# Kernel tuning notes

Hardware: AMD Instinct MI355X
Metric: run time of the kernel (lower is better)

## Reference

```python
import jax, jax.numpy as jnp
import numpy as np

N = 50000   # nodes
E = 800000  # edges
IN = 128
H = 256
OUT = 10
G = 128     # graphs in batch


def _uniform(key, shape, fan_in):
    bound = 1.0 / np.sqrt(fan_in)
    return jax.random.uniform(key, shape, jnp.float32, -bound, bound)


def setup_inputs() -> dict:
    key = jax.random.key(0)
    ks = jax.random.split(key, 12)
    x = jax.random.normal(ks[0], (N, IN), jnp.float32)
    edge_index = jax.random.randint(ks[1], (2, E), 0, N, dtype=jnp.int64)
    edge_weight = jax.random.uniform(ks[2], (E,), jnp.float32)
    batch = jnp.sort(jax.random.randint(ks[3], (N,), 0, G, dtype=jnp.int64))
    # GCNConv weights (bias=False)
    W0 = _uniform(ks[4], (IN, H), IN)
    W1 = _uniform(ks[5], (H, H), H)
    W2 = _uniform(ks[6], (H, H), H)
    # MLP head: [H, H, OUT]
    Wm1 = _uniform(ks[7], (H, H), H)
    bm1 = _uniform(ks[8], (H,), H)
    Wm2 = _uniform(ks[9], (H, OUT), H)
    bm2 = _uniform(ks[10], (OUT,), H)
    return dict(x=x, edge_index=edge_index, edge_weight=edge_weight, batch=batch,
                W0=W0, W1=W1, W2=W2, Wm1=Wm1, bm1=bm1, Wm2=Wm2, bm2=bm2)


def _gcn_conv(h, W, row, col, dinv_sqrt):
    """GCNConv with self-loops and symmetric deg^-1/2 normalization, bias=False.
    Self-loop contribution handled analytically (norm = dinv_sqrt[i]^2)."""
    hw = h @ W                                        # [N, H]
    norm = dinv_sqrt[row] * dinv_sqrt[col]            # [E]
    msg = hw[row] * norm[:, None]                     # [E, H] gather-scale
    agg = jax.ops.segment_sum(msg, col, num_segments=N)  # scatter-add at targets
    return agg + (dinv_sqrt * dinv_sqrt)[:, None] * hw    # add self-loop term


def reference(x, edge_index, edge_weight, batch, W0, W1, W2, Wm1, bm1, Wm2, bm2):
    row, col = edge_index[0], edge_index[1]
    # degree including self-loop (edge_weight is ignored, as in the source)
    deg = jax.ops.segment_sum(jnp.ones((E,), x.dtype), col, num_segments=N) + 1.0
    dinv_sqrt = jax.lax.rsqrt(deg)
    h = x
    for W in (W0, W1, W2):
        h = jax.nn.relu(_gcn_conv(h, W, row, col, dinv_sqrt))
    # global mean pool over graphs
    counts = jax.ops.segment_sum(jnp.ones((N,), h.dtype), batch, num_segments=G)
    pooled = jax.ops.segment_sum(h, batch, num_segments=G) / jnp.maximum(counts, 1.0)[:, None]
    # MLP head (dropout inactive at inference)
    hmid = jax.nn.relu(pooled @ Wm1 + bm1)
    last = hmid @ Wm2 + bm2
    return jax.nn.log_softmax(last, axis=-1), jax.nn.sigmoid(last), last
```

## Files before the change

### kernel.cpp

```cpp
#include <hip/hip_runtime.h>
#include <math.h>

#define N_NODES 50000
#define N_PAD   50048
#define N_EDGES 800000
#define CSR_CAP 1200000
#define IN_F 128
#define H_F 256
#define OUT_F 10
#define N_G 128
#define POOL_CHUNK 128
#define POOL_MAXCHUNKS 16
#define NCHUNKS 196

typedef __attribute__((ext_vector_type(4))) float f32x4;
typedef __attribute__((ext_vector_type(2))) float f32x2;
typedef unsigned char u8;

__device__ inline f32x2 fp8x2_f32_lo(unsigned int v) {
    return __builtin_amdgcn_cvt_pk_f32_fp8(v, false);
}
__device__ inline f32x2 fp8x2_f32_hi(unsigned int v) {
    return __builtin_amdgcn_cvt_pk_f32_fp8(v, true);
}
__device__ inline unsigned int f32_fp8x2_lo(float a, float b, unsigned int old) {
    return __builtin_amdgcn_cvt_pk_fp8_f32(a, b, old, false);
}
__device__ inline unsigned int f32_fp8x2_hi(float a, float b, unsigned int old) {
    return __builtin_amdgcn_cvt_pk_fp8_f32(a, b, old, true);
}
__device__ inline u8 f32_fp8(float a) {
    return (u8)(f32_fp8x2_lo(a, a, 0u) & 0xff);
}
__device__ inline ushort f2bf(float x) {
    union { float f; unsigned int u; } v; v.f = x;
    unsigned int r = v.u + 0x7fff + ((v.u >> 16) & 1);
    return (ushort)(r >> 16);
}
__device__ inline float bf2f(ushort u) {
    union { unsigned int u; float f; } v; v.u = ((unsigned int)u) << 16; return v.f;
}

__device__ inline void gl2lds16(const void* g, void* l) {
    __builtin_amdgcn_global_load_lds(
        (const __attribute__((address_space(1))) unsigned int*)g,
        (__attribute__((address_space(3))) unsigned int*)l,
        16, 0, 0);
}

#define PREP_HIST 782
#define PREP_X   (PREP_HIST + 6250)
#define PREP_T0  (PREP_X + 128)
#define PREP_T1  (PREP_T0 + 256)
#define PREP_T2  (PREP_T1 + 256)
#define PREP_GS  (PREP_T2 + NCHUNKS)

__global__ __launch_bounds__(256) void prep_kernel(
    const int* __restrict__ col, int* __restrict__ counts,
    int* __restrict__ rank,
    const float* __restrict__ x, u8* __restrict__ xb,
    const float* __restrict__ W0, u8* __restrict__ W0t,
    const float* __restrict__ W1, u8* __restrict__ W1t,
    const float* __restrict__ W2, u8* __restrict__ W2t,
    const int* __restrict__ batch, int* __restrict__ gstart) {
    int b = blockIdx.x;
    int tid = threadIdx.x;
    if (b < PREP_HIST) {
        int base = b * 1024 + tid;
        int c[4];
        #pragma unroll
        for (int u = 0; u < 4; ++u) {
            int e = base + u * 256;
            c[u] = (e < N_EDGES) ? col[e] : -1;
        }
        int rk[4];
        #pragma unroll
        for (int u = 0; u < 4; ++u)
            if (c[u] >= 0) rk[u] = atomicAdd(&counts[c[u]], 1);
        #pragma unroll
        for (int u = 0; u < 4; ++u)
            if (c[u] >= 0) rank[base + u * 256] = rk[u];
    } else if (b < PREP_X) {
        int i = (b - PREP_HIST) * 256 + tid;
        float4 v = *(const float4*)(x + (size_t)i * 4);
        unsigned int p = f32_fp8x2_lo(v.x, v.y, 0u);
        p = f32_fp8x2_hi(v.z, v.w, p);
        *(unsigned int*)(xb + (size_t)i * 4) = p;
    } else if (b < PREP_T0) {
        int idx = (b - PREP_X) * 256 + tid;
        int k = idx >> 8, nn = idx & 255;
        W0t[nn * IN_F + k] = f32_fp8(W0[idx]);
    } else if (b < PREP_T1) {
        int idx = (b - PREP_T0) * 256 + tid;
        int k = idx >> 8, nn = idx & 255;
        W1t[nn * H_F + k] = f32_fp8(W1[idx]);
    } else if (b < PREP_T2) {
        int idx = (b - PREP_T1) * 256 + tid;
        int k = idx >> 8, nn = idx & 255;
        W2t[nn * H_F + k] = f32_fp8(W2[idx]);
    } else {
        int i = (b - PREP_T2) * 256 + tid;
        if (i >= N_NODES) return;
        int bb = batch[i];
        if (i == 0) {
            for (int g = 0; g <= bb; ++g) gstart[g] = 0;
        } else {
            int p = batch[i - 1];
            if (p != bb) { for (int g = p + 1; g <= bb; ++g) gstart[g] = i; }
        }
        if (i == N_NODES - 1) {
            for (int g = bb + 1; g <= N_G; ++g) gstart[g] = N_NODES;
        }
    }
}

__global__ __launch_bounds__(256) void chunk_reduce(const int* __restrict__ counts,
                                                    int* __restrict__ csum,
                                                    float* __restrict__ pooled, int n) {
    if (blockIdx.x < 128) pooled[blockIdx.x * 256 + threadIdx.x] = 0.f;
    int i = blockIdx.x * 256 + threadIdx.x;
    int v = (i < n) ? ((counts[i] + 7) & ~7) : 0;
    #pragma unroll
    for (int off = 32; off; off >>= 1) v += __shfl_down(v, off);
    __shared__ int ws[4];
    if ((threadIdx.x & 63) == 0) ws[threadIdx.x >> 6] = v;
    __syncthreads();
    if (threadIdx.x == 0) csum[blockIdx.x] = ws[0] + ws[1] + ws[2] + ws[3];
}

__global__ __launch_bounds__(256) void scan_dinv_kernel(const int* __restrict__ counts,
                                                        const int* __restrict__ csum,
                                                        int* __restrict__ offsets,
                                                        float* __restrict__ dinv,
                                                        unsigned int* __restrict__ csr_ew,
                                                        int n) {
    int tid = threadIdx.x;
    int lane = tid & 63, wid = tid >> 6;
    int cv = (tid < NCHUNKS) ? csum[tid] : 0;
    int xc = cv;
    #pragma unroll
    for (int off = 1; off < 64; off <<= 1) {
        int t = __shfl_up(xc, off);
        if (lane >= off) xc += t;
    }
    __shared__ int cw[4], cpre[4];
    __shared__ int cexcl[257];
    if (lane == 63) cw[wid] = xc;
    __syncthreads();
    if (tid == 0) { int s = 0; for (int k = 0; k < 4; ++k) { cpre[k] = s; s += cw[k]; } }
    __syncthreads();
    cexcl[tid] = cpre[wid] + xc - cv;
    if (tid == 255) cexcl[256] = cpre[3] + cw[3];
    __syncthreads();
    int base = cexcl[blockIdx.x];
    int i = blockIdx.x * 256 + tid;
    int v = (i < n) ? counts[i] : 0;
    int pv = (v + 7) & ~7;
    int x = pv;
    #pragma unroll
    for (int off = 1; off < 64; off <<= 1) {
        int t = __shfl_up(x, off);
        if (lane >= off) x += t;
    }
    __shared__ int wsum[4], wpre[4];
    if (lane == 63) wsum[wid] = x;
    __syncthreads();
    if (tid == 0) { int s = 0; for (int k = 0; k < 4; ++k) { wpre[k] = s; s += wsum[k]; } }
    __syncthreads();
    if (i < n) {
        int o = base + wpre[wid] + x - pv;
        offsets[i] = o;
        dinv[i] = rsqrtf((float)(v + 1));
        for (int z = v; z < pv; ++z) csr_ew[o + z] = 0u;
    }
    if (blockIdx.x == 0 && tid == 0) offsets[n] = cexcl[NCHUNKS];
}

__global__ __launch_bounds__(256) void fill_csr_kernel(const int* __restrict__ row,
                                                       const int* __restrict__ col,
                                                       const int* __restrict__ offsets,
                                                       const int* __restrict__ rank,
                                                       const float* __restrict__ dinv,
                                                       unsigned int* __restrict__ csr_ew) {
    int e0 = blockIdx.x * 512 + threadIdx.x;
    int e1 = e0 + 256;
    int c0 = -1, c1 = -1, r0 = 0, r1 = 0, k0 = 0, k1 = 0;
    if (e0 < N_EDGES) { c0 = col[e0]; r0 = row[e0]; k0 = rank[e0]; }
    if (e1 < N_EDGES) { c1 = col[e1]; r1 = row[e1]; k1 = rank[e1]; }
    float dc0 = 0.f, dr0 = 0.f, dc1 = 0.f, dr1 = 0.f;
    if (c0 >= 0) { dc0 = dinv[c0]; dr0 = dinv[r0]; }
    if (c1 >= 0) { dc1 = dinv[c1]; dr1 = dinv[r1]; }
    if (c0 >= 0)
        csr_ew[offsets[c0] + k0] = (unsigned int)r0 | ((unsigned int)f2bf(dc0 * dr0) << 16);
    if (c1 >= 0)
        csr_ew[offsets[c1] + k1] = (unsigned int)r1 | ((unsigned int)f2bf(dc1 * dr1) << 16);
}

template <int K, bool RELU>
__global__ __launch_bounds__(256) void gemm_fp8(const u8* __restrict__ A,
                                                const u8* __restrict__ Bt,
                                                u8* __restrict__ C) {
    __shared__ u8 As[4 * 4096];
    __shared__ u8 Bs[4 * 4096];
    int tid = threadIdx.x;
    int lane = tid & 63;
    int w = tid >> 6;
    int wm = w & 1, wn = w >> 1;
    int l16 = lane & 15, quad = lane >> 4;
    int row0 = blockIdx.x * 128;
    int col0 = blockIdx.y * 128;
    f32x4 acc[4][4] = {};

    int sr = tid >> 1;
    int sh = (tid & 1) * 16;
    const u8* ga = A + (size_t)(row0 + sr) * K + sh;
    const u8* gb = Bt + (size_t)(col0 + sr) * K + sh;

    #pragma unroll
    for (int k0 = 0; k0 < K; k0 += 128) {
        if (k0) __syncthreads();
        #pragma unroll
        for (int q = 0; q < 4; ++q) {
            gl2lds16(ga + k0 + q * 32, As + q * 4096 + w * 1024);
            gl2lds16(gb + k0 + q * 32, Bs + q * 4096 + w * 1024);
        }
        __syncthreads();
        #pragma unroll
        for (int h = 0; h < 4; ++h) {
            long af[4], bfr[4];
            #pragma unroll
            for (int i = 0; i < 4; ++i)
                af[i] = *(const long*)&As[h * 4096 + (wm * 64 + i * 16 + l16) * 32 + quad * 8];
            #pragma unroll
            for (int j = 0; j < 4; ++j)
                bfr[j] = *(const long*)&Bs[h * 4096 + (wn * 64 + j * 16 + l16) * 32 + quad * 8];
            #pragma unroll
            for (int i = 0; i < 4; ++i)
                #pragma unroll
                for (int j = 0; j < 4; ++j)
                    acc[i][j] = __builtin_amdgcn_mfma_f32_16x16x32_fp8_fp8(af[i], bfr[j], acc[i][j], 0, 0, 0);
        }
    }
    #pragma unroll
    for (int i = 0; i < 4; ++i) {
        int rowb = row0 + wm * 64 + i * 16 + quad * 4;
        #pragma unroll
        for (int r = 0; r < 4; ++r) {
            int grow = rowb + r;
            #pragma unroll
            for (int j = 0; j < 4; ++j) {
                int gcol = col0 + wn * 64 + j * 16 + l16;
                float v = acc[i][j][r];
                if (RELU) v = fmaxf(v, 0.f);
                C[(size_t)grow * H_F + gcol] = f32_fp8(v);
            }
        }
    }
}

__global__ __launch_bounds__(256) void aggregate128(const u8* __restrict__ hw,
                                                    const float* __restrict__ dinv,
                                                    const int* __restrict__ offsets,
                                                    const unsigned int* __restrict__ csr_ew,
                                                    u8* __restrict__ hout) {
    int w = threadIdx.x >> 6;
    int lane = threadIdx.x & 63;
    int i = blockIdx.x * 4 + w;
    if (i >= N_NODES) return;
    float di = dinv[i];
    const u8* base = hw + (size_t)lane * 2;
    unsigned int su = *(const unsigned short*)(base + (size_t)i * IN_F);
    f32x2 sv = fp8x2_f32_lo(su);
    float s = di * di;
    float a0 = s * sv.x, a1 = s * sv.y;
    int t = __builtin_amdgcn_readfirstlane(offsets[i]);
    int end = __builtin_amdgcn_readfirstlane(offsets[i + 1]);
    if (t < end) {
        uint4 eA = *(const uint4*)(csr_ew + t);
        uint4 eB = *(const uint4*)(csr_ew + t + 4);
        for (; t < end; t += 8) {
            uint4 nA, nB;
            if (t + 8 < end) {
                nA = *(const uint4*)(csr_ew + t + 8);
                nB = *(const uint4*)(csr_ew + t + 12);
            }
            unsigned int e[8] = {eA.x, eA.y, eA.z, eA.w, eB.x, eB.y, eB.z, eB.w};
            unsigned int v[8];
            #pragma unroll
            for (int u = 0; u < 8; ++u)
                v[u] = *(const unsigned short*)(base + (size_t)(e[u] & 0xffff) * IN_F);
            #pragma unroll
            for (int u = 0; u < 8; ++u) {
                float wq = bf2f((ushort)(e[u] >> 16));
                f32x2 f = fp8x2_f32_lo(v[u]);
                a0 += wq * f.x; a1 += wq * f.y;
            }
            eA = nA; eB = nB;
        }
    }
    unsigned int o = f32_fp8x2_lo(a0, a1, 0u);
    *(unsigned short*)(hout + (size_t)i * IN_F + lane * 2) = (unsigned short)(o & 0xffff);
}

__global__ __launch_bounds__(256) void aggregate256(const u8* __restrict__ hw,
                                                    const float* __restrict__ dinv,
                                                    const int* __restrict__ offsets,
                                                    const unsigned int* __restrict__ csr_ew,
                                                    u8* __restrict__ hout) {
    int w = threadIdx.x >> 6;
    int lane = threadIdx.x & 63;
    int i = blockIdx.x * 4 + w;
    if (i >= N_NODES) return;
    float di = dinv[i];
    const u8* base = hw + (size_t)lane * 4;
    unsigned int su = *(const unsigned int*)(base + (size_t)i * H_F);
    f32x2 slo = fp8x2_f32_lo(su), shi = fp8x2_f32_hi(su);
    float s = di * di;
    float a0 = s * slo.x, a1 = s * slo.y, a2 = s * shi.x, a3 = s * shi.y;
    int t = __builtin_amdgcn_readfirstlane(offsets[i]);
    int end = __builtin_amdgcn_readfirstlane(offsets[i + 1]);
    if (t < end) {
        uint4 eA = *(const uint4*)(csr_ew + t);
        uint4 eB = *(const uint4*)(csr_ew + t + 4);
        for (; t < end; t += 8) {
            uint4 nA, nB;
            if (t + 8 < end) {
                nA = *(const uint4*)(csr_ew + t + 8);
                nB = *(const uint4*)(csr_ew + t + 12);
            }
            unsigned int e[8] = {eA.x, eA.y, eA.z, eA.w, eB.x, eB.y, eB.z, eB.w};
            unsigned int v[8];
            #pragma unroll
            for (int u = 0; u < 8; ++u)
                v[u] = *(const unsigned int*)(base + (size_t)(e[u] & 0xffff) * H_F);
            #pragma unroll
            for (int u = 0; u < 8; ++u) {
                float wq = bf2f((ushort)(e[u] >> 16));
                f32x2 lo = fp8x2_f32_lo(v[u]), hi = fp8x2_f32_hi(v[u]);
                a0 += wq * lo.x; a1 += wq * lo.y;
                a2 += wq * hi.x; a3 += wq * hi.y;
            }
            eA = nA; eB = nB;
        }
    }
    unsigned int o = f32_fp8x2_lo(fmaxf(a0, 0.f), fmaxf(a1, 0.f), 0u);
    o = f32_fp8x2_hi(fmaxf(a2, 0.f), fmaxf(a3, 0.f), o);
    *(unsigned int*)(hout + (size_t)i * H_F + lane * 4) = o;
}

__global__ __launch_bounds__(256) void pool_part(const u8* __restrict__ h,
                                                 const int* __restrict__ gstart,
                                                 float* __restrict__ pooled) {
    int g = blockIdx.x;
    int s = gstart[g] + blockIdx.y * POOL_CHUNK;
    int e = min(gstart[g + 1], s + POOL_CHUNK);
    if (s >= e) return;
    int w = threadIdx.x >> 6;
    int lane = threadIdx.x & 63;
    float a0 = 0.f, a1 = 0.f, a2 = 0.f, a3 = 0.f;
    for (int i = s + w; i < e; i += 4) {
        unsigned int v = *(const unsigned int*)(h + (size_t)i * H_F + lane * 4);
        f32x2 lo = fp8x2_f32_lo(v), hi = fp8x2_f32_hi(v);
        a0 += lo.x; a1 += lo.y; a2 += hi.x; a3 += hi.y;
    }
    __shared__ float sm[4][H_F];
    *(f32x4*)&sm[w][lane * 4] = (f32x4){a0, a1, a2, a3};
    __syncthreads();
    int t = threadIdx.x;
    float tot = sm[0][t] + sm[1][t] + sm[2][t] + sm[3][t];
    atomicAdd(&pooled[g * H_F + t], tot);
}

__global__ __launch_bounds__(256) void mlp_head_kernel(const float* __restrict__ pooled,
                                                       const int* __restrict__ gstart,
                                                       const float* __restrict__ Wm1,
                                                       const float* __restrict__ bm1,
                                                       const float* __restrict__ Wm2,
                                                       const float* __restrict__ bm2,
                                                       float* __restrict__ out) {
    __shared__ float p[H_F];
    __shared__ float h[H_F];
    __shared__ float lastv[OUT_F];
    __shared__ float stats[2];
    int g = blockIdx.x, j = threadIdx.x;
    int cnt = gstart[g + 1] - gstart[g];
    p[j] = pooled[g * H_F + j] / (float)max(cnt, 1);
    __syncthreads();
    float acc = bm1[j];
    for (int k = 0; k < H_F; ++k) acc += p[k] * Wm1[k * H_F + j];
    h[j] = fmaxf(acc, 0.f);
    __syncthreads();
    if (j < OUT_F) {
        float a = bm2[j];
        for (int k = 0; k < H_F; ++k) a += h[k] * Wm2[k * OUT_F + j];
        lastv[j] = a;
    }
    __syncthreads();
    if (j == 0) {
        float m = -1e30f;
        for (int o = 0; o < OUT_F; ++o) m = fmaxf(m, lastv[o]);
        float s = 0.f;
        for (int o = 0; o < OUT_F; ++o) s += expf(lastv[o] - m);
        stats[0] = m; stats[1] = logf(s);
    }
    __syncthreads();
    if (j < OUT_F) {
        float v = lastv[j];
        out[g * OUT_F + j] = v - stats[0] - stats[1];
        out[(size_t)N_G * OUT_F + g * OUT_F + j] = 1.f / (1.f + expf(-v));
        out[(size_t)2 * N_G * OUT_F + g * OUT_F + j] = v;
    }
}

extern "C" void kernel_launch(void* const* d_in, const int* in_sizes, int n_in,
                              void* d_out, int out_size, void* d_ws, size_t ws_size,
                              hipStream_t stream) {
    const float* x   = (const float*)d_in[0];
    const int* edge_index = (const int*)d_in[1];
    const int* batch = (const int*)d_in[3];
    const float* W0  = (const float*)d_in[4];
    const float* W1  = (const float*)d_in[5];
    const float* W2  = (const float*)d_in[6];
    const float* Wm1 = (const float*)d_in[7];
    const float* bm1 = (const float*)d_in[8];
    const float* Wm2 = (const float*)d_in[9];
    const float* bm2 = (const float*)d_in[10];
    float* out = (float*)d_out;

    char* ws = (char*)d_ws;
    size_t off = 0;
    auto alloc = [&](size_t bytes) -> void* {
        void* p = ws + off; off += (bytes + 255) & ~(size_t)255; return p;
    };
    u8* xb       = (u8*)alloc((size_t)N_PAD * IN_F);
    u8* bufA     = (u8*)alloc((size_t)N_PAD * H_F);
    u8* bufB     = (u8*)alloc((size_t)N_PAD * H_F);
    u8* t0       = (u8*)alloc((size_t)N_PAD * IN_F);
    u8* W0t      = (u8*)alloc((size_t)H_F * IN_F);
    u8* W1t      = (u8*)alloc((size_t)H_F * H_F);
    u8* W2t      = (u8*)alloc((size_t)H_F * H_F);
    float* dinv    = (float*)alloc((size_t)N_NODES * 4);
    int*   counts  = (int*)alloc((size_t)N_NODES * 4);
    int*   offsets = (int*)alloc((size_t)(N_NODES + 1) * 4);
    int*   rank    = (int*)alloc((size_t)N_EDGES * 4);
    unsigned int* csr_ew = (unsigned int*)alloc((size_t)CSR_CAP * 4);
    int*   csum    = (int*)alloc((size_t)256 * 4);
    int*   gstart  = (int*)alloc((size_t)(N_G + 1) * 4);
    float* pooled  = (float*)alloc((size_t)N_G * H_F * 4);

    const int* row = edge_index;
    const int* col = edge_index + N_EDGES;

    hipMemsetAsync(counts, 0, (size_t)N_NODES * 4, stream);

    prep_kernel<<<PREP_GS, 256, 0, stream>>>(col, counts, rank, x, xb, W0, W0t,
                                             W1, W1t, W2, W2t, batch, gstart);
    chunk_reduce<<<NCHUNKS, 256, 0, stream>>>(counts, csum, pooled, N_NODES);
    scan_dinv_kernel<<<NCHUNKS, 256, 0, stream>>>(counts, csum, offsets, dinv,
                                                  csr_ew, N_NODES);
    fill_csr_kernel<<<1563, 256, 0, stream>>>(row, col, offsets, rank, dinv, csr_ew);

    dim3 gg(N_PAD / 128, H_F / 128);
    int agg_blocks = (N_NODES + 3) / 4;
    aggregate128<<<agg_blocks, 256, 0, stream>>>(xb, dinv, offsets, csr_ew, t0);
    gemm_fp8<IN_F, true><<<gg, 256, 0, stream>>>(t0, W0t, bufA);
    gemm_fp8<H_F, false><<<gg, 256, 0, stream>>>(bufA, W1t, bufB);
    aggregate256<<<agg_blocks, 256, 0, stream>>>(bufB, dinv, offsets, csr_ew, bufA);
    gemm_fp8<H_F, false><<<gg, 256, 0, stream>>>(bufA, W2t, bufB);
    aggregate256<<<agg_blocks, 256, 0, stream>>>(bufB, dinv, offsets, csr_ew, bufA);

    dim3 pg(N_G, POOL_MAXCHUNKS);
    pool_part<<<pg, 256, 0, stream>>>(bufA, gstart, pooled);
    mlp_head_kernel<<<N_G, 256, 0, stream>>>(pooled, gstart, Wm1, bm1, Wm2, bm2, out);
}
```

Baseline: 291.2 us.

## Fuse pooling into MLP head and drop separate chunk-reduce scan pass

Removes the chunk_reduce kernel: each scan block now computes its own base offset by summing all preceding padded counts directly, trading a launch for redundant reads (up to 50K ints per block). The pooling and MLP head are merged into one kernel with one block per graph, which removes the pooled buffer, its atomics and zeroing, and one launch. The cost is that pooling parallelism drops from up to 16 chunks per graph to a single block per graph of roughly 390 nodes.

Result: slower. 326.1 us (+12.0%).

```diff
diff --git a/kernel.cpp b/kernel.cpp
--- a/kernel.cpp
+++ b/kernel.cpp
@@ -9,8 +9,6 @@
 #define H_F 256
 #define OUT_F 10
 #define N_G 128
-#define POOL_CHUNK 128
-#define POOL_MAXCHUNKS 16
 #define NCHUNKS 196
 
 typedef __attribute__((ext_vector_type(4))) float f32x4;
@@ -114,46 +112,26 @@
     }
 }
 
-__global__ __launch_bounds__(256) void chunk_reduce(const int* __restrict__ counts,
-                                                    int* __restrict__ csum,
-                                                    float* __restrict__ pooled, int n) {
-    if (blockIdx.x < 128) pooled[blockIdx.x * 256 + threadIdx.x] = 0.f;
-    int i = blockIdx.x * 256 + threadIdx.x;
-    int v = (i < n) ? ((counts[i] + 7) & ~7) : 0;
-    #pragma unroll
-    for (int off = 32; off; off >>= 1) v += __shfl_down(v, off);
-    __shared__ int ws[4];
-    if ((threadIdx.x & 63) == 0) ws[threadIdx.x >> 6] = v;
-    __syncthreads();
-    if (threadIdx.x == 0) csum[blockIdx.x] = ws[0] + ws[1] + ws[2] + ws[3];
-}
-
 __global__ __launch_bounds__(256) void scan_dinv_kernel(const int* __restrict__ counts,
-                                                        const int* __restrict__ csum,
                                                         int* __restrict__ offsets,
                                                         float* __restrict__ dinv,
                                                         unsigned int* __restrict__ csr_ew,
                                                         int n) {
     int tid = threadIdx.x;
     int lane = tid & 63, wid = tid >> 6;
-    int cv = (tid < NCHUNKS) ? csum[tid] : 0;
-    int xc = cv;
+    int limit = blockIdx.x * 256;
+    int pre = 0;
+    for (int j = tid; j < limit; j += 256) pre += (counts[j] + 7) & ~7;
     #pragma unroll
-    for (int off = 1; off < 64; off <<= 1) {
-        int t = __shfl_up(xc, off);
-        if (lane >= off) xc += t;
-    }
-    __shared__ int cw[4], cpre[4];
-    __shared__ int cexcl[257];
-    if (lane == 63) cw[wid] = xc;
-    __syncthreads();
-    if (tid == 0) { int s = 0; for (int k = 0; k < 4; ++k) { cpre[k] = s; s += cw[k]; } }
-    __syncthreads();
-    cexcl[tid] = cpre[wid] + xc - cv;
-    if (tid == 255) cexcl[256] = cpre[3] + cw[3];
-    __syncthreads();
-    int base = cexcl[blockIdx.x];
-    int i = blockIdx.x * 256 + tid;
+    for (int off = 32; off; off >>= 1) pre += __shfl_down(pre, off);
+    __shared__ int bw[4];
+    __shared__ int basev;
+    if (lane == 0) bw[wid] = pre;
+    __syncthreads();
+    if (tid == 0) basev = bw[0] + bw[1] + bw[2] + bw[3];
+    __syncthreads();
+    int base = basev;
+    int i = limit + tid;
     int v = (i < n) ? counts[i] : 0;
     int pv = (v + 7) & ~7;
     int x = pv;
@@ -173,7 +151,8 @@
         dinv[i] = rsqrtf((float)(v + 1));
         for (int z = v; z < pv; ++z) csr_ew[o + z] = 0u;
     }
-    if (blockIdx.x == 0 && tid == 0) offsets[n] = cexcl[NCHUNKS];
+    if (blockIdx.x == NCHUNKS - 1 && tid == 0)
+        offsets[n] = base + wpre[3] + wsum[3];
 }
 
 __global__ __launch_bounds__(256) void fill_csr_kernel(const int* __restrict__ row,
@@ -348,13 +327,20 @@
     *(unsigned int*)(hout + (size_t)i * H_F + lane * 4) = o;
 }
 
-__global__ __launch_bounds__(256) void pool_part(const u8* __restrict__ h,
-                                                 const int* __restrict__ gstart,
-                                                 float* __restrict__ pooled) {
+__global__ __launch_bounds__(256) void pool_mlp_kernel(const u8* __restrict__ h,
+                                                       const int* __restrict__ gstart,
+                                                       const float* __restrict__ Wm1,
+                                                       const float* __restrict__ bm1,
+                                                       const float* __restrict__ Wm2,
+                                                       const float* __restrict__ bm2,
+                                                       float* __restrict__ out) {
+    __shared__ float sm[4][H_F];
+    __shared__ float p[H_F];
+    __shared__ float hmid[H_F];
+    __shared__ float lastv[OUT_F];
+    __shared__ float stats[2];
     int g = blockIdx.x;
-    int s = gstart[g] + blockIdx.y * POOL_CHUNK;
-    int e = min(gstart[g + 1], s + POOL_CHUNK);
-    if (s >= e) return;
+    int s = gstart[g], e = gstart[g + 1];
     int w = threadIdx.x >> 6;
     int lane = threadIdx.x & 63;
     float a0 = 0.f, a1 = 0.f, a2 = 0.f, a3 = 0.f;
@@ -363,45 +349,28 @@
         f32x2 lo = fp8x2_f32_lo(v), hi = fp8x2_f32_hi(v);
         a0 += lo.x; a1 += lo.y; a2 += hi.x; a3 += hi.y;
     }
-    __shared__ float sm[4][H_F];
     *(f32x4*)&sm[w][lane * 4] = (f32x4){a0, a1, a2, a3};
     __syncthreads();
-    int t = threadIdx.x;
-    float tot = sm[0][t] + sm[1][t] + sm[2][t] + sm[3][t];
-    atomicAdd(&pooled[g * H_F + t], tot);
-}
-
-__global__ __launch_bounds__(256) void mlp_head_kernel(const float* __restrict__ pooled,
-                                                       const int* __restrict__ gstart,
-                                                       const float* __restrict__ Wm1,
-                                                       const float* __restrict__ bm1,
-                                                       const float* __restrict__ Wm2,
-                                                       const float* __restrict__ bm2,
-                                                       float* __restrict__ out) {
-    __shared__ float p[H_F];
-    __shared__ float h[H_F];
-    __shared__ float lastv[OUT_F];
-    __shared__ float stats[2];
-    int g = blockIdx.x, j = threadIdx.x;
-    int cnt = gstart[g + 1] - gstart[g];
-    p[j] = pooled[g * H_F + j] / (float)max(cnt, 1);
+    int j = threadIdx.x;
+    int cnt = e - s;
+    p[j] = (sm[0][j] + sm[1][j] + sm[2][j] + sm[3][j]) / (float)max(cnt, 1);
     __syncthreads();
     float acc = bm1[j];
     for (int k = 0; k < H_F; ++k) acc += p[k] * Wm1[k * H_F + j];
-    h[j] = fmaxf(acc, 0.f);
+    hmid[j] = fmaxf(acc, 0.f);
     __syncthreads();
     if (j < OUT_F) {
         float a = bm2[j];
-        for (int k = 0; k < H_F; ++k) a += h[k] * Wm2[k * OUT_F + j];
+        for (int k = 0; k < H_F; ++k) a += hmid[k] * Wm2[k * OUT_F + j];
         lastv[j] = a;
     }
     __syncthreads();
     if (j == 0) {
         float m = -1e30f;
         for (int o = 0; o < OUT_F; ++o) m = fmaxf(m, lastv[o]);
-        float s = 0.f;
-        for (int o = 0; o < OUT_F; ++o) s += expf(lastv[o] - m);
-        stats[0] = m; stats[1] = logf(s);
+        float sxp = 0.f;
+        for (int o = 0; o < OUT_F; ++o) sxp += expf(lastv[o] - m);
+        stats[0] = m; stats[1] = logf(sxp);
     }
     __syncthreads();
     if (j < OUT_F) {
@@ -444,9 +413,7 @@
     int*   offsets = (int*)alloc((size_t)(N_NODES + 1) * 4);
     int*   rank    = (int*)alloc((size_t)N_EDGES * 4);
     unsigned int* csr_ew = (unsigned int*)alloc((size_t)CSR_CAP * 4);
-    int*   csum    = (int*)alloc((size_t)256 * 4);
     int*   gstart  = (int*)alloc((size_t)(N_G + 1) * 4);
-    float* pooled  = (float*)alloc((size_t)N_G * H_F * 4);
 
     const int* row = edge_index;
     const int* col = edge_index + N_EDGES;
@@ -455,8 +422,7 @@
 
     prep_kernel<<<PREP_GS, 256, 0, stream>>>(col, counts, rank, x, xb, W0, W0t,
                                              W1, W1t, W2, W2t, batch, gstart);
-    chunk_reduce<<<NCHUNKS, 256, 0, stream>>>(counts, csum, pooled, N_NODES);
-    scan_dinv_kernel<<<NCHUNKS, 256, 0, stream>>>(counts, csum, offsets, dinv,
+    scan_dinv_kernel<<<NCHUNKS, 256, 0, stream>>>(counts, offsets, dinv,
                                                   csr_ew, N_NODES);
     fill_csr_kernel<<<1563, 256, 0, stream>>>(row, col, offsets, rank, dinv, csr_ew);
 
@@ -469,7 +435,5 @@
     gemm_fp8<H_F, false><<<gg, 256, 0, stream>>>(bufA, W2t, bufB);
     aggregate256<<<agg_blocks, 256, 0, stream>>>(bufB, dinv, offsets, csr_ew, bufA);
 
-    dim3 pg(N_G, POOL_MAXCHUNKS);
-    pool_part<<<pg, 256, 0, stream>>>(bufA, gstart, pooled);
-    mlp_head_kernel<<<N_G, 256, 0, stream>>>(pooled, gstart, Wm1, bm1, Wm2, bm2, out);
-}
+    pool_mlp_kernel<<<N_G, 256, 0, stream>>>(bufA, gstart, Wm1, bm1, Wm2, bm2, out);
+}
```
